# Kernel tuning notes

Measured on AMD Instinct MI355X. Metric: run time of the kernel, lower is better.

## Reference

```python
import jax, jax.numpy as jnp
import numpy as np

N_NODES = 100000
N_EDGES = 600000
IN_SIZE = 128
OUT_SIZE = 128
N_GRAPHS = 100
BN_EPS = 1e-5


def setup_inputs() -> dict:
    key = jax.random.key(0)
    ks = jax.random.split(key, 8)
    h = jax.random.normal(ks[0], (N_NODES, IN_SIZE), dtype=jnp.float32)
    norm = jax.random.uniform(ks[1], (N_NODES, 1), dtype=jnp.float32)
    src = jax.random.randint(ks[2], (N_EDGES,), 0, N_NODES, dtype=jnp.int32)
    dst = jax.random.randint(ks[3], (N_EDGES,), 0, N_NODES, dtype=jnp.int32)
    graph_ids = jnp.sort(jax.random.randint(ks[4], (N_NODES,), 0, N_GRAPHS, dtype=jnp.int32))
    # Linear + BatchNorm params
    W = jax.random.normal(ks[5], (IN_SIZE, OUT_SIZE), dtype=jnp.float32) / np.sqrt(IN_SIZE)
    b = jnp.zeros((OUT_SIZE,), dtype=jnp.float32)
    gamma = jnp.ones((OUT_SIZE,), dtype=jnp.float32)
    beta = jnp.zeros((OUT_SIZE,), dtype=jnp.float32)
    return {"h": h, "norm": norm, "W": W, "b": b, "gamma": gamma, "beta": beta,
            "src": src, "dst": dst, "graph_ids": graph_ids}


def reference(h, norm, W, b, gamma, beta, src, dst, graph_ids):
    # pre-normalize, scatter-sum over edges (copy_src + sum), post-normalize
    x = h * norm                                            # [N, in]
    agg = jax.ops.segment_sum(x[src], dst, num_segments=N_NODES)  # SpMM
    x = agg * norm
    # linear + relu
    x = jax.nn.relu(jnp.dot(x, W) + b)                      # [N, out]
    # BatchNorm1d (training-mode: batch mean, biased variance)
    mean = jnp.mean(x, axis=0)
    var = jnp.mean(jnp.square(x - mean), axis=0)
    x = (x - mean) * jax.lax.rsqrt(var + BN_EPS) * gamma + beta
    # sum_nodes pooling per graph
    phis = jax.ops.segment_sum(x, graph_ids, num_segments=N_GRAPHS)  # [G, out]
    return (x, phis)
```

## Files before the change

kernel.cpp:

```cpp
#include <hip/hip_runtime.h>
#include <hip/hip_bf16.h>

#define N_NODES 100000
#define N_PAD 100096
#define N_EDGES 600000
#define CH 128
#define N_GRAPHS 100
#define BN_EPS 1e-5f
#define NBUCKET 64
#define CAP 32
#define OVFCAP 8192
#define FILL_BLOCKS 586
#define PRESCALE_BLOCKS 6250

typedef __bf16 bf16x8 __attribute__((ext_vector_type(8)));
typedef float f32x4 __attribute__((ext_vector_type(4)));

__device__ __forceinline__ ushort f2bf(float f) {
    union { float f; unsigned u; } x; x.f = f;
    unsigned u = x.u;
    unsigned r = (u + 0x7fffu + ((u >> 16) & 1u)) >> 16;
    return (ushort)r;
}
__device__ __forceinline__ float bflo(unsigned p) { return __builtin_bit_cast(float, p << 16); }
__device__ __forceinline__ float bfhi(unsigned p) { return __builtin_bit_cast(float, p & 0xffff0000u); }

__global__ __launch_bounds__(256) void k_front(const int* __restrict__ src,
        const int* __restrict__ dst, const float* __restrict__ h,
        const float* __restrict__ norm, const float* __restrict__ W,
        int* __restrict__ cnt, int* __restrict__ ovfcur, int* __restrict__ ovf,
        int* __restrict__ esrc, ushort* __restrict__ xh, ushort* __restrict__ Wt) {
    unsigned bid = blockIdx.x;
    if (bid < FILL_BLOCKS) {
        int e0 = (bid * 256 + threadIdx.x) * 4;
        if (e0 < N_EDGES) {
            int4 d = *(const int4*)(dst + e0);
            int4 s = *(const int4*)(src + e0);
            int s0 = atomicAdd(&cnt[d.x], 1);
            int s1 = atomicAdd(&cnt[d.y], 1);
            int s2 = atomicAdd(&cnt[d.z], 1);
            int s3 = atomicAdd(&cnt[d.w], 1);
            if (s0 < CAP) esrc[d.x * CAP + s0] = s.x;
            else { int p = atomicAdd(ovfcur, 1); if (p < OVFCAP) { ovf[2*p] = d.x; ovf[2*p+1] = s.x; } }
            if (s1 < CAP) esrc[d.y * CAP + s1] = s.y;
            else { int p = atomicAdd(ovfcur, 1); if (p < OVFCAP) { ovf[2*p] = d.y; ovf[2*p+1] = s.y; } }
            if (s2 < CAP) esrc[d.z * CAP + s2] = s.z;
            else { int p = atomicAdd(ovfcur, 1); if (p < OVFCAP) { ovf[2*p] = d.z; ovf[2*p+1] = s.z; } }
            if (s3 < CAP) esrc[d.w * CAP + s3] = s.w;
            else { int p = atomicAdd(ovfcur, 1); if (p < OVFCAP) { ovf[2*p] = d.w; ovf[2*p+1] = s.w; } }
        }
    } else if (bid < FILL_BLOCKS + PRESCALE_BLOCKS) {
        int t = (bid - FILL_BLOCKS) * 256 + threadIdx.x;
        int n = t >> 4, c = (t & 15) << 3;
        float nm = norm[n];
        float4 a = *(const float4*)(h + (size_t)n * CH + c);
        float4 d = *(const float4*)(h + (size_t)n * CH + c + 4);
        uint4 o;
        o.x = (unsigned)f2bf(a.x * nm) | ((unsigned)f2bf(a.y * nm) << 16);
        o.y = (unsigned)f2bf(a.z * nm) | ((unsigned)f2bf(a.w * nm) << 16);
        o.z = (unsigned)f2bf(d.x * nm) | ((unsigned)f2bf(d.y * nm) << 16);
        o.w = (unsigned)f2bf(d.z * nm) | ((unsigned)f2bf(d.w * nm) << 16);
        *(uint4*)(xh + (size_t)n * CH + c) = o;
    } else {
        int t = (bid - FILL_BLOCKS - PRESCALE_BLOCKS) * 256 + threadIdx.x;
        int k = t >> 7, o = t & 127;
        Wt[o * CH + k] = f2bf(W[t]);
    }
}

__global__ __launch_bounds__(256) void k_gather(const ushort* __restrict__ xh,
        const float* __restrict__ norm, const int* __restrict__ cnt,
        const int* __restrict__ esrc, const int* __restrict__ ovfcur,
        const int* __restrict__ ovf, ushort* __restrict__ x2) {
    int t = blockIdx.x * 256 + threadIdx.x;
    int n = t >> 4;
    int c = (t & 15) << 3;
    if (n >= N_PAD) return;
    int e = 0;
    float nn = 0.f;
    if (n < N_NODES) { e = min(cnt[n], CAP); nn = norm[n]; }
    int base = n * CAP;
    float a0=0.f,a1=0.f,a2=0.f,a3=0.f,a4=0.f,a5=0.f,a6=0.f,a7=0.f;
    int j = 0;
    for (; j + 4 <= e; j += 4) {
        int s0 = esrc[base + j], s1 = esrc[base + j + 1];
        int s2 = esrc[base + j + 2], s3 = esrc[base + j + 3];
        uint4 v0 = *(const uint4*)(xh + (size_t)s0 * CH + c);
        uint4 v1 = *(const uint4*)(xh + (size_t)s1 * CH + c);
        uint4 v2 = *(const uint4*)(xh + (size_t)s2 * CH + c);
        uint4 v3 = *(const uint4*)(xh + (size_t)s3 * CH + c);
        a0 += bflo(v0.x) + bflo(v1.x) + bflo(v2.x) + bflo(v3.x);
        a1 += bfhi(v0.x) + bfhi(v1.x) + bfhi(v2.x) + bfhi(v3.x);
        a2 += bflo(v0.y) + bflo(v1.y) + bflo(v2.y) + bflo(v3.y);
        a3 += bfhi(v0.y) + bfhi(v1.y) + bfhi(v2.y) + bfhi(v3.y);
        a4 += bflo(v0.z) + bflo(v1.z) + bflo(v2.z) + bflo(v3.z);
        a5 += bfhi(v0.z) + bfhi(v1.z) + bfhi(v2.z) + bfhi(v3.z);
        a6 += bflo(v0.w) + bflo(v1.w) + bflo(v2.w) + bflo(v3.w);
        a7 += bfhi(v0.w) + bfhi(v1.w) + bfhi(v2.w) + bfhi(v3.w);
    }
    for (; j < e; j++) {
        int s = esrc[base + j];
        uint4 v = *(const uint4*)(xh + (size_t)s * CH + c);
        a0 += bflo(v.x); a1 += bfhi(v.x);
        a2 += bflo(v.y); a3 += bfhi(v.y);
        a4 += bflo(v.z); a5 += bfhi(v.z);
        a6 += bflo(v.w); a7 += bfhi(v.w);
    }
    if (n < N_NODES) {
        int no = *ovfcur;
        if (no > 0) {
            no = min(no, OVFCAP);
            for (int i = 0; i < no; i++) {
                if (ovf[2*i] == n) {
                    int s = ovf[2*i+1];
                    uint4 v = *(const uint4*)(xh + (size_t)s * CH + c);
                    a0 += bflo(v.x); a1 += bfhi(v.x);
                    a2 += bflo(v.y); a3 += bfhi(v.y);
                    a4 += bflo(v.z); a5 += bfhi(v.z);
                    a6 += bflo(v.w); a7 += bfhi(v.w);
                }
            }
        }
    }
    uint4 o;
    o.x = (unsigned)f2bf(a0 * nn) | ((unsigned)f2bf(a1 * nn) << 16);
    o.y = (unsigned)f2bf(a2 * nn) | ((unsigned)f2bf(a3 * nn) << 16);
    o.z = (unsigned)f2bf(a4 * nn) | ((unsigned)f2bf(a5 * nn) << 16);
    o.w = (unsigned)f2bf(a6 * nn) | ((unsigned)f2bf(a7 * nn) << 16);
    *(uint4*)(x2 + (size_t)n * CH + c) = o;
}

__global__ __launch_bounds__(256) void k_gemm(const ushort* __restrict__ x2,
        const ushort* __restrict__ Wt, const float* __restrict__ bias,
        ushort* __restrict__ y16, float* __restrict__ psum, float* __restrict__ psq) {
    __shared__ ushort ys[128 * CH];

    int tid = threadIdx.x;
    int w = tid >> 6, L = tid & 63;
    int c15 = L & 15, quad = L >> 4;
    size_t nb = (size_t)blockIdx.x * 128 + w * 32;

    const bf16x8* A0 = (const bf16x8*)(x2 + (nb + c15) * CH);
    const bf16x8* A1 = (const bf16x8*)(x2 + (nb + 16 + c15) * CH);

    f32x4 acc0[8] = {}, acc1[8] = {};
    #pragma unroll
    for (int kt = 0; kt < 4; kt++) {
        bf16x8 a0 = A0[kt * 4 + quad];
        bf16x8 a1 = A1[kt * 4 + quad];
        #pragma unroll
        for (int ot = 0; ot < 8; ot++) {
            bf16x8 b = *(const bf16x8*)(Wt + (size_t)(ot * 16 + c15) * CH + kt * 32 + quad * 8);
            acc0[ot] = __builtin_amdgcn_mfma_f32_16x16x32_bf16(a0, b, acc0[ot], 0, 0, 0);
            acc1[ot] = __builtin_amdgcn_mfma_f32_16x16x32_bf16(a1, b, acc1[ot], 0, 0, 0);
        }
    }

    float sA[8], qA[8];
    #pragma unroll
    for (int ot = 0; ot < 8; ot++) {
        int col = ot * 16 + c15;
        float bv = bias[col];
        float s_ = 0.f, q_ = 0.f;
        #pragma unroll
        for (int r = 0; r < 4; r++) {
            size_t n = nb + quad * 4 + r;
            float v = fmaxf(acc0[ot][r] + bv, 0.f);
            ys[(w * 32 + quad * 4 + r) * CH + col] = f2bf(v);
            if (n < N_NODES) { s_ += v; q_ += v * v; }
            size_t n2 = n + 16;
            float v2 = fmaxf(acc1[ot][r] + bv, 0.f);
            ys[(w * 32 + 16 + quad * 4 + r) * CH + col] = f2bf(v2);
            if (n2 < N_NODES) { s_ += v2; q_ += v2 * v2; }
        }
        sA[ot] = s_; qA[ot] = q_;
    }
    __syncthreads();

    {
        const uint4* ysv = (const uint4*)ys;
        uint4* out = (uint4*)(y16 + (size_t)blockIdx.x * 128 * CH);
        #pragma unroll
        for (int i = 0; i < 8; i++) out[tid + i * 256] = ysv[tid + i * 256];
    }
    __syncthreads();

    float* red = (float*)ys;
    #pragma unroll
    for (int ot = 0; ot < 8; ot++) {
        red[ot * 256 + tid] = sA[ot];
        red[2048 + ot * 256 + tid] = qA[ot];
    }
    __syncthreads();

    if (tid < 128) {
        int ot = tid >> 4, cc = tid & 15;
        int col = ot * 16 + cc;
        float S = 0.f, Q = 0.f;
        #pragma unroll
        for (int g = 0; g < 16; g++) {
            int sl = (g >> 2) * 64 + (g & 3) * 16 + cc;
            S += red[ot * 256 + sl];
            Q += red[2048 + ot * 256 + sl];
        }
        int bucket = blockIdx.x & (NBUCKET - 1);
        atomicAdd(&psum[bucket * CH + col], S);
        atomicAdd(&psq[bucket * CH + col], Q);
    }
}

__global__ void k_finalize(const float* __restrict__ psum, const float* __restrict__ psq,
        const float* __restrict__ gamma, const float* __restrict__ beta,
        float* __restrict__ scale, float* __restrict__ shift, float* __restrict__ phis) {
    int t = threadIdx.x;
    float S = 0.f, Q = 0.f;
    for (int g = 0; g < NBUCKET; g++) { S += psum[g * CH + t]; Q += psq[g * CH + t]; }
    const float invN = 1.f / (float)N_NODES;
    float mean = S * invN;
    float var  = Q * invN - mean * mean;
    float sc   = gamma[t] * rsqrtf(var + BN_EPS);
    scale[t] = sc;
    shift[t] = beta[t] - mean * sc;
    for (int i = t; i < N_GRAPHS * CH; i += 128) phis[i] = 0.f;
}

__global__ __launch_bounds__(256) void k_bnpool(const ushort* __restrict__ y16,
        const int* __restrict__ gids, const float* __restrict__ scale,
        const float* __restrict__ shift, float* __restrict__ xout,
        float* __restrict__ phis) {
    __shared__ float smP[16][CH];

    int tid = threadIdx.x;
    int cg = tid & 15, rl = tid >> 4;
    int c = cg * 8;
    int r0 = blockIdx.x * 256;
    int rbase = r0 + rl * 16;

    float4 sc0 = *(const float4*)(scale + c), sc1 = *(const float4*)(scale + c + 4);
    float4 sh0 = *(const float4*)(shift + c), sh1 = *(const float4*)(shift + c + 4);

    bool fast = (r0 + 255 < N_NODES) && (gids[r0] == gids[r0 + 255]);

    if (fast) {
        float4 p0 = make_float4(0.f,0.f,0.f,0.f), p1 = make_float4(0.f,0.f,0.f,0.f);
        for (int j = 0; j < 16; j++) {
            int r = rbase + j;
            uint4 v = *(const uint4*)(y16 + (size_t)r * CH + c);
            float4 f0, f1;
            f0.x = fmaf(bflo(v.x), sc0.x, sh0.x); f0.y = fmaf(bfhi(v.x), sc0.y, sh0.y);
            f0.z = fmaf(bflo(v.y), sc0.z, sh0.z); f0.w = fmaf(bfhi(v.y), sc0.w, sh0.w);
            f1.x = fmaf(bflo(v.z), sc1.x, sh1.x); f1.y = fmaf(bfhi(v.z), sc1.y, sh1.y);
            f1.z = fmaf(bflo(v.w), sc1.z, sh1.z); f1.w = fmaf(bfhi(v.w), sc1.w, sh1.w);
            *(float4*)(xout + (size_t)r * CH + c) = f0;
            *(float4*)(xout + (size_t)r * CH + c + 4) = f1;
            p0.x += f0.x; p0.y += f0.y; p0.z += f0.z; p0.w += f0.w;
            p1.x += f1.x; p1.y += f1.y; p1.z += f1.z; p1.w += f1.w;
        }
        *(float4*)&smP[rl][c] = p0;
        *(float4*)&smP[rl][c + 4] = p1;
        __syncthreads();
        if (tid < 128) {
            int g = gids[r0];
            float S = 0.f;
            #pragma unroll
            for (int k = 0; k < 16; k++) S += smP[k][tid];
            atomicAdd(&phis[(size_t)g * CH + tid], S);
        }
    } else {
        float p[8] = {};
        int gprev = -1;
        for (int j = 0; j < 16; j++) {
            int r = rbase + j;
            if (r >= N_NODES) break;
            int g = gids[r];
            if (g != gprev) {
                if (gprev >= 0) {
                    #pragma unroll
                    for (int k = 0; k < 8; k++) {
                        atomicAdd(&phis[(size_t)gprev * CH + c + k], p[k]);
                        p[k] = 0.f;
                    }
                }
                gprev = g;
            }
            uint4 v = *(const uint4*)(y16 + (size_t)r * CH + c);
            float f[8];
            f[0] = fmaf(bflo(v.x), sc0.x, sh0.x); f[1] = fmaf(bfhi(v.x), sc0.y, sh0.y);
            f[2] = fmaf(bflo(v.y), sc0.z, sh0.z); f[3] = fmaf(bfhi(v.y), sc0.w, sh0.w);
            f[4] = fmaf(bflo(v.z), sc1.x, sh1.x); f[5] = fmaf(bfhi(v.z), sc1.y, sh1.y);
            f[6] = fmaf(bflo(v.w), sc1.z, sh1.z); f[7] = fmaf(bfhi(v.w), sc1.w, sh1.w);
            *(float4*)(xout + (size_t)r * CH + c) = make_float4(f[0], f[1], f[2], f[3]);
            *(float4*)(xout + (size_t)r * CH + c + 4) = make_float4(f[4], f[5], f[6], f[7]);
            #pragma unroll
            for (int k = 0; k < 8; k++) p[k] += f[k];
        }
        if (gprev >= 0) {
            #pragma unroll
            for (int k = 0; k < 8; k++)
                atomicAdd(&phis[(size_t)gprev * CH + c + k], p[k]);
        }
    }
}

extern "C" void kernel_launch(void* const* d_in, const int* in_sizes, int n_in,
                              void* d_out, int out_size, void* d_ws, size_t ws_size,
                              hipStream_t stream)
{
    const float* h     = (const float*)d_in[0];
    const float* norm  = (const float*)d_in[1];
    const float* W     = (const float*)d_in[2];
    const float* b     = (const float*)d_in[3];
    const float* gamma = (const float*)d_in[4];
    const float* beta  = (const float*)d_in[5];
    const int*   src   = (const int*)d_in[6];
    const int*   dst   = (const int*)d_in[7];
    const int*   gids  = (const int*)d_in[8];

    float* x_out = (float*)d_out;
    float* phis  = x_out + (size_t)N_NODES * CH;

    ushort* xh   = (ushort*)d_ws;
    ushort* x2   = xh + (size_t)N_NODES * CH;
    ushort* y16  = x2 + (size_t)N_PAD * CH;
    ushort* Wt   = y16 + (size_t)N_PAD * CH;
    int*   cnt     = (int*)(Wt + CH * CH);
    float* psum    = (float*)(cnt + N_NODES);
    float* psq     = psum + NBUCKET * CH;
    int*   ovfcur  = (int*)(psq + NBUCKET * CH);
    int*   esrc    = ovfcur + 4;
    int*   ovf     = esrc + (size_t)N_NODES * CAP;
    float* scale   = (float*)(ovf + 2 * OVFCAP);
    float* shift   = scale + CH;

    hipMemsetAsync(cnt, 0, (size_t)(N_NODES + 2 * NBUCKET * CH + 4) * sizeof(int), stream);

    k_front<<<FILL_BLOCKS + PRESCALE_BLOCKS + 64, 256, 0, stream>>>(
        src, dst, h, norm, W, cnt, ovfcur, ovf, esrc, xh, Wt);
    k_gather<<<N_PAD / 16, 256, 0, stream>>>(xh, norm, cnt, esrc, ovfcur, ovf, x2);
    k_gemm<<<N_PAD / 128, 256, 0, stream>>>(x2, Wt, b, y16, psum, psq);
    k_finalize<<<1, 128, 0, stream>>>(psum, psq, gamma, beta, scale, shift, phis);
    k_bnpool<<<(N_NODES + 255) / 256, 256, 0, stream>>>(y16, gids, scale, shift, x_out, phis);
}
```

Before: 229.2 us.

## Apply linear layer before aggregation and fuse gather with bias, ReLU and BN stats

```diff
diff --git a/kernel.cpp b/kernel.cpp
--- a/kernel.cpp
+++ b/kernel.cpp
@@ -8,10 +8,13 @@
 #define N_GRAPHS 100
 #define BN_EPS 1e-5f
 #define NBUCKET 64
-#define CAP 32
+#define CAP 16
 #define OVFCAP 8192
 #define FILL_BLOCKS 586
-#define PRESCALE_BLOCKS 6250
+#define GEMM_BLOCKS 782
+#define GATHER_BLOCKS 1024
+#define ZERO_INTS (N_NODES + 2 * NBUCKET * CH + 4)
+#define ZERO_BLOCKS 455
 
 typedef __bf16 bf16x8 __attribute__((ext_vector_type(8)));
 typedef float f32x4 __attribute__((ext_vector_type(4)));
@@ -25,14 +28,47 @@
 __device__ __forceinline__ float bflo(unsigned p) { return __builtin_bit_cast(float, p << 16); }
 __device__ __forceinline__ float bfhi(unsigned p) { return __builtin_bit_cast(float, p & 0xffff0000u); }
 
+__global__ __launch_bounds__(256) void k_prep(const float* __restrict__ W,
+        int* __restrict__ zbase, ushort* __restrict__ Wt) {
+    unsigned bid = blockIdx.x;
+    if (bid < ZERO_BLOCKS) {
+        int i = bid * 256 + threadIdx.x;
+        if (i < ZERO_INTS) zbase[i] = 0;
+    } else {
+        int t = (bid - ZERO_BLOCKS) * 256 + threadIdx.x;
+        int k = t >> 7, o = t & 127;
+        Wt[o * CH + k] = f2bf(W[t]);
+    }
+}
+
+__device__ __forceinline__ bf16x8 mk_a(const float* __restrict__ hrow, int k,
+                                       float nm, bool valid) {
+    union { bf16x8 v; ushort u[8]; } r;
+    if (valid) {
+        float4 p = *(const float4*)(hrow + k);
+        float4 q = *(const float4*)(hrow + k + 4);
+        r.u[0] = f2bf(p.x * nm); r.u[1] = f2bf(p.y * nm);
+        r.u[2] = f2bf(p.z * nm); r.u[3] = f2bf(p.w * nm);
+        r.u[4] = f2bf(q.x * nm); r.u[5] = f2bf(q.y * nm);
+        r.u[6] = f2bf(q.z * nm); r.u[7] = f2bf(q.w * nm);
+    } else {
+        #pragma unroll
+        for (int i = 0; i < 8; i++) r.u[i] = 0;
+    }
+    return r.v;
+}
+
 __global__ __launch_bounds__(256) void k_front(const int* __restrict__ src,
         const int* __restrict__ dst, const float* __restrict__ h,
-        const float* __restrict__ norm, const float* __restrict__ W,
+        const float* __restrict__ norm, const ushort* __restrict__ Wt,
         int* __restrict__ cnt, int* __restrict__ ovfcur, int* __restrict__ ovf,
-        int* __restrict__ esrc, ushort* __restrict__ xh, ushort* __restrict__ Wt) {
+        int* __restrict__ esrc, ushort* __restrict__ z16) {
+    __shared__ ushort ys[128 * CH];
     unsigned bid = blockIdx.x;
+    int tid = threadIdx.x;
+
     if (bid < FILL_BLOCKS) {
-        int e0 = (bid * 256 + threadIdx.x) * 4;
+        int e0 = (bid * 256 + tid) * 4;
         if (e0 < N_EDGES) {
             int4 d = *(const int4*)(dst + e0);
             int4 s = *(const int4*)(src + e0);
@@ -49,71 +85,100 @@
             if (s3 < CAP) esrc[d.w * CAP + s3] = s.w;
             else { int p = atomicAdd(ovfcur, 1); if (p < OVFCAP) { ovf[2*p] = d.w; ovf[2*p+1] = s.w; } }
         }
-    } else if (bid < FILL_BLOCKS + PRESCALE_BLOCKS) {
-        int t = (bid - FILL_BLOCKS) * 256 + threadIdx.x;
-        int n = t >> 4, c = (t & 15) << 3;
-        float nm = norm[n];
-        float4 a = *(const float4*)(h + (size_t)n * CH + c);
-        float4 d = *(const float4*)(h + (size_t)n * CH + c + 4);
-        uint4 o;
-        o.x = (unsigned)f2bf(a.x * nm) | ((unsigned)f2bf(a.y * nm) << 16);
-        o.y = (unsigned)f2bf(a.z * nm) | ((unsigned)f2bf(a.w * nm) << 16);
-        o.z = (unsigned)f2bf(d.x * nm) | ((unsigned)f2bf(d.y * nm) << 16);
-        o.w = (unsigned)f2bf(d.z * nm) | ((unsigned)f2bf(d.w * nm) << 16);
-        *(uint4*)(xh + (size_t)n * CH + c) = o;
-    } else {
-        int t = (bid - FILL_BLOCKS - PRESCALE_BLOCKS) * 256 + threadIdx.x;
-        int k = t >> 7, o = t & 127;
-        Wt[o * CH + k] = f2bf(W[t]);
-    }
-}
-
-__global__ __launch_bounds__(256) void k_gather(const ushort* __restrict__ xh,
+        return;
+    }
+
+    int gb = bid - FILL_BLOCKS;
+    int w = tid >> 6, L = tid & 63;
+    int c15 = L & 15, quad = L >> 4;
+    int nb = gb * 128 + w * 32;
+    int r0 = nb + c15, r1 = nb + 16 + c15;
+    bool v0r = r0 < N_NODES, v1r = r1 < N_NODES;
+    float nm0 = v0r ? norm[r0] : 0.f;
+    float nm1 = v1r ? norm[r1] : 0.f;
+    const float* h0 = h + (size_t)r0 * CH;
+    const float* h1 = h + (size_t)r1 * CH;
+
+    f32x4 acc0[8] = {}, acc1[8] = {};
+    #pragma unroll
+    for (int kt = 0; kt < 4; kt++) {
+        int k = kt * 32 + quad * 8;
+        bf16x8 a0 = mk_a(h0, k, nm0, v0r);
+        bf16x8 a1 = mk_a(h1, k, nm1, v1r);
+        #pragma unroll
+        for (int ot = 0; ot < 8; ot++) {
+            bf16x8 b = *(const bf16x8*)(Wt + (size_t)(ot * 16 + c15) * CH + k);
+            acc0[ot] = __builtin_amdgcn_mfma_f32_16x16x32_bf16(a0, b, acc0[ot], 0, 0, 0);
+            acc1[ot] = __builtin_amdgcn_mfma_f32_16x16x32_bf16(a1, b, acc1[ot], 0, 0, 0);
+        }
+    }
+
+    #pragma unroll
+    for (int ot = 0; ot < 8; ot++) {
+        int col = ot * 16 + c15;
+        #pragma unroll
+        for (int r = 0; r < 4; r++) {
+            ys[(w * 32 + quad * 4 + r) * CH + col] = f2bf(acc0[ot][r]);
+            ys[(w * 32 + 16 + quad * 4 + r) * CH + col] = f2bf(acc1[ot][r]);
+        }
+    }
+    __syncthreads();
+    {
+        const uint4* ysv = (const uint4*)ys;
+        uint4* out = (uint4*)(z16 + (size_t)gb * 128 * CH);
+        #pragma unroll
+        for (int i = 0; i < 8; i++) out[tid + i * 256] = ysv[tid + i * 256];
+    }
+}
+
+__global__ __launch_bounds__(256) void k_gather(const ushort* __restrict__ z16,
         const float* __restrict__ norm, const int* __restrict__ cnt,
         const int* __restrict__ esrc, const int* __restrict__ ovfcur,
-        const int* __restrict__ ovf, ushort* __restrict__ x2) {
-    int t = blockIdx.x * 256 + threadIdx.x;
-    int n = t >> 4;
-    int c = (t & 15) << 3;
-    if (n >= N_PAD) return;
-    int e = 0;
-    float nn = 0.f;
-    if (n < N_NODES) { e = min(cnt[n], CAP); nn = norm[n]; }
-    int base = n * CAP;
-    float a0=0.f,a1=0.f,a2=0.f,a3=0.f,a4=0.f,a5=0.f,a6=0.f,a7=0.f;
-    int j = 0;
-    for (; j + 4 <= e; j += 4) {
-        int s0 = esrc[base + j], s1 = esrc[base + j + 1];
-        int s2 = esrc[base + j + 2], s3 = esrc[base + j + 3];
-        uint4 v0 = *(const uint4*)(xh + (size_t)s0 * CH + c);
-        uint4 v1 = *(const uint4*)(xh + (size_t)s1 * CH + c);
-        uint4 v2 = *(const uint4*)(xh + (size_t)s2 * CH + c);
-        uint4 v3 = *(const uint4*)(xh + (size_t)s3 * CH + c);
-        a0 += bflo(v0.x) + bflo(v1.x) + bflo(v2.x) + bflo(v3.x);
-        a1 += bfhi(v0.x) + bfhi(v1.x) + bfhi(v2.x) + bfhi(v3.x);
-        a2 += bflo(v0.y) + bflo(v1.y) + bflo(v2.y) + bflo(v3.y);
-        a3 += bfhi(v0.y) + bfhi(v1.y) + bfhi(v2.y) + bfhi(v3.y);
-        a4 += bflo(v0.z) + bflo(v1.z) + bflo(v2.z) + bflo(v3.z);
-        a5 += bfhi(v0.z) + bfhi(v1.z) + bfhi(v2.z) + bfhi(v3.z);
-        a6 += bflo(v0.w) + bflo(v1.w) + bflo(v2.w) + bflo(v3.w);
-        a7 += bfhi(v0.w) + bfhi(v1.w) + bfhi(v2.w) + bfhi(v3.w);
-    }
-    for (; j < e; j++) {
-        int s = esrc[base + j];
-        uint4 v = *(const uint4*)(xh + (size_t)s * CH + c);
-        a0 += bflo(v.x); a1 += bfhi(v.x);
-        a2 += bflo(v.y); a3 += bfhi(v.y);
-        a4 += bflo(v.z); a5 += bfhi(v.z);
-        a6 += bflo(v.w); a7 += bfhi(v.w);
-    }
-    if (n < N_NODES) {
-        int no = *ovfcur;
+        const int* __restrict__ ovf, const float* __restrict__ bias,
+        ushort* __restrict__ y16, float* __restrict__ psum, float* __restrict__ psq) {
+    __shared__ float sred[2][16][CH];
+
+    int tid = threadIdx.x;
+    int cg = tid & 15, rl = tid >> 4;
+    int c = cg * 8;
+    float4 b0 = *(const float4*)(bias + c), b1 = *(const float4*)(bias + c + 4);
+    float s8[8] = {}, q8[8] = {};
+    int no = min(*ovfcur, OVFCAP);
+
+    for (int n = blockIdx.x * 16 + rl; n < N_NODES; n += GATHER_BLOCKS * 16) {
+        int e = min(cnt[n], CAP);
+        float nn = norm[n];
+        int base = n * CAP;
+        float a0=0.f,a1=0.f,a2=0.f,a3=0.f,a4=0.f,a5=0.f,a6=0.f,a7=0.f;
+        int j = 0;
+        for (; j + 4 <= e; j += 4) {
+            int4 s4 = *(const int4*)(esrc + base + j);
+            uint4 v0 = *(const uint4*)(z16 + (size_t)s4.x * CH + c);
+            uint4 v1 = *(const uint4*)(z16 + (size_t)s4.y * CH + c);
+            uint4 v2 = *(const uint4*)(z16 + (size_t)s4.z * CH + c);
+            uint4 v3 = *(const uint4*)(z16 + (size_t)s4.w * CH + c);
+            a0 += bflo(v0.x) + bflo(v1.x) + bflo(v2.x) + bflo(v3.x);
+            a1 += bfhi(v0.x) + bfhi(v1.x) + bfhi(v2.x) + bfhi(v3.x);
+            a2 += bflo(v0.y) + bflo(v1.y) + bflo(v2.y) + bflo(v3.y);
+            a3 += bfhi(v0.y) + bfhi(v1.y) + bfhi(v2.y) + bfhi(v3.y);
+            a4 += bflo(v0.z) + bflo(v1.z) + bflo(v2.z) + bflo(v3.z);
+            a5 += bfhi(v0.z) + bfhi(v1.z) + bfhi(v2.z) + bfhi(v3.z);
+            a6 += bflo(v0.w) + bflo(v1.w) + bflo(v2.w) + bflo(v3.w);
+            a7 += bfhi(v0.w) + bfhi(v1.w) + bfhi(v2.w) + bfhi(v3.w);
+        }
+        for (; j < e; j++) {
+            int s = esrc[base + j];
+            uint4 v = *(const uint4*)(z16 + (size_t)s * CH + c);
+            a0 += bflo(v.x); a1 += bfhi(v.x);
+            a2 += bflo(v.y); a3 += bfhi(v.y);
+            a4 += bflo(v.z); a5 += bfhi(v.z);
+            a6 += bflo(v.w); a7 += bfhi(v.w);
+        }
         if (no > 0) {
-            no = min(no, OVFCAP);
             for (int i = 0; i < no; i++) {
                 if (ovf[2*i] == n) {
                     int s = ovf[2*i+1];
-                    uint4 v = *(const uint4*)(xh + (size_t)s * CH + c);
+                    uint4 v = *(const uint4*)(z16 + (size_t)s * CH + c);
                     a0 += bflo(v.x); a1 += bfhi(v.x);
                     a2 += bflo(v.y); a3 += bfhi(v.y);
                     a4 += bflo(v.z); a5 += bfhi(v.z);
@@ -121,91 +186,37 @@
                 }
             }
         }
-    }
-    uint4 o;
-    o.x = (unsigned)f2bf(a0 * nn) | ((unsigned)f2bf(a1 * nn) << 16);
-    o.y = (unsigned)f2bf(a2 * nn) | ((unsigned)f2bf(a3 * nn) << 16);
-    o.z = (unsigned)f2bf(a4 * nn) | ((unsigned)f2bf(a5 * nn) << 16);
-    o.w = (unsigned)f2bf(a6 * nn) | ((unsigned)f2bf(a7 * nn) << 16);
-    *(uint4*)(x2 + (size_t)n * CH + c) = o;
-}
-
-__global__ __launch_bounds__(256) void k_gemm(const ushort* __restrict__ x2,
-        const ushort* __restrict__ Wt, const float* __restrict__ bias,
-        ushort* __restrict__ y16, float* __restrict__ psum, float* __restrict__ psq) {
-    __shared__ ushort ys[128 * CH];
-
-    int tid = threadIdx.x;
-    int w = tid >> 6, L = tid & 63;
-    int c15 = L & 15, quad = L >> 4;
-    size_t nb = (size_t)blockIdx.x * 128 + w * 32;
-
-    const bf16x8* A0 = (const bf16x8*)(x2 + (nb + c15) * CH);
-    const bf16x8* A1 = (const bf16x8*)(x2 + (nb + 16 + c15) * CH);
-
-    f32x4 acc0[8] = {}, acc1[8] = {};
-    #pragma unroll
-    for (int kt = 0; kt < 4; kt++) {
-        bf16x8 a0 = A0[kt * 4 + quad];
-        bf16x8 a1 = A1[kt * 4 + quad];
-        #pragma unroll
-        for (int ot = 0; ot < 8; ot++) {
-            bf16x8 b = *(const bf16x8*)(Wt + (size_t)(ot * 16 + c15) * CH + kt * 32 + quad * 8);
-            acc0[ot] = __builtin_amdgcn_mfma_f32_16x16x32_bf16(a0, b, acc0[ot], 0, 0, 0);
-            acc1[ot] = __builtin_amdgcn_mfma_f32_16x16x32_bf16(a1, b, acc1[ot], 0, 0, 0);
-        }
-    }
-
-    float sA[8], qA[8];
-    #pragma unroll
-    for (int ot = 0; ot < 8; ot++) {
-        int col = ot * 16 + c15;
-        float bv = bias[col];
-        float s_ = 0.f, q_ = 0.f;
-        #pragma unroll
-        for (int r = 0; r < 4; r++) {
-            size_t n = nb + quad * 4 + r;
-            float v = fmaxf(acc0[ot][r] + bv, 0.f);
-            ys[(w * 32 + quad * 4 + r) * CH + col] = f2bf(v);
-            if (n < N_NODES) { s_ += v; q_ += v * v; }
-            size_t n2 = n + 16;
-            float v2 = fmaxf(acc1[ot][r] + bv, 0.f);
-            ys[(w * 32 + 16 + quad * 4 + r) * CH + col] = f2bf(v2);
-            if (n2 < N_NODES) { s_ += v2; q_ += v2 * v2; }
-        }
-        sA[ot] = s_; qA[ot] = q_;
-    }
+        float f[8];
+        f[0] = fmaxf(fmaf(a0, nn, b0.x), 0.f);
+        f[1] = fmaxf(fmaf(a1, nn, b0.y), 0.f);
+        f[2] = fmaxf(fmaf(a2, nn, b0.z), 0.f);
+        f[3] = fmaxf(fmaf(a3, nn, b0.w), 0.f);
+        f[4] = fmaxf(fmaf(a4, nn, b1.x), 0.f);
+        f[5] = fmaxf(fmaf(a5, nn, b1.y), 0.f);
+        f[6] = fmaxf(fmaf(a6, nn, b1.z), 0.f);
+        f[7] = fmaxf(fmaf(a7, nn, b1.w), 0.f);
+        uint4 o;
+        o.x = (unsigned)f2bf(f[0]) | ((unsigned)f2bf(f[1]) << 16);
+        o.y = (unsigned)f2bf(f[2]) | ((unsigned)f2bf(f[3]) << 16);
+        o.z = (unsigned)f2bf(f[4]) | ((unsigned)f2bf(f[5]) << 16);
+        o.w = (unsigned)f2bf(f[6]) | ((unsigned)f2bf(f[7]) << 16);
+        *(uint4*)(y16 + (size_t)n * CH + c) = o;
+        #pragma unroll
+        for (int k = 0; k < 8; k++) { s8[k] += f[k]; q8[k] += f[k] * f[k]; }
+    }
+
+    *(float4*)&sred[0][rl][c]     = make_float4(s8[0], s8[1], s8[2], s8[3]);
+    *(float4*)&sred[0][rl][c + 4] = make_float4(s8[4], s8[5], s8[6], s8[7]);
+    *(float4*)&sred[1][rl][c]     = make_float4(q8[0], q8[1], q8[2], q8[3]);
+    *(float4*)&sred[1][rl][c + 4] = make_float4(q8[4], q8[5], q8[6], q8[7]);
     __syncthreads();
-
-    {
-        const uint4* ysv = (const uint4*)ys;
-        uint4* out = (uint4*)(y16 + (size_t)blockIdx.x * 128 * CH);
-        #pragma unroll
-        for (int i = 0; i < 8; i++) out[tid + i * 256] = ysv[tid + i * 256];
-    }
-    __syncthreads();
-
-    float* red = (float*)ys;
-    #pragma unroll
-    for (int ot = 0; ot < 8; ot++) {
-        red[ot * 256 + tid] = sA[ot];
-        red[2048 + ot * 256 + tid] = qA[ot];
-    }
-    __syncthreads();
-
     if (tid < 128) {
-        int ot = tid >> 4, cc = tid & 15;
-        int col = ot * 16 + cc;
         float S = 0.f, Q = 0.f;
         #pragma unroll
-        for (int g = 0; g < 16; g++) {
-            int sl = (g >> 2) * 64 + (g & 3) * 16 + cc;
-            S += red[ot * 256 + sl];
-            Q += red[2048 + ot * 256 + sl];
-        }
+        for (int k = 0; k < 16; k++) { S += sred[0][k][tid]; Q += sred[1][k][tid]; }
         int bucket = blockIdx.x & (NBUCKET - 1);
-        atomicAdd(&psum[bucket * CH + col], S);
-        atomicAdd(&psq[bucket * CH + col], Q);
+        atomicAdd(&psum[bucket * CH + tid], S);
+        atomicAdd(&psq[bucket * CH + tid], Q);
     }
 }
 
@@ -319,9 +330,8 @@
     float* x_out = (float*)d_out;
     float* phis  = x_out + (size_t)N_NODES * CH;
 
-    ushort* xh   = (ushort*)d_ws;
-    ushort* x2   = xh + (size_t)N_NODES * CH;
-    ushort* y16  = x2 + (size_t)N_PAD * CH;
+    ushort* z16  = (ushort*)d_ws;
+    ushort* y16  = z16 + (size_t)N_PAD * CH;
     ushort* Wt   = y16 + (size_t)N_PAD * CH;
     int*   cnt     = (int*)(Wt + CH * CH);
     float* psum    = (float*)(cnt + N_NODES);
@@ -332,12 +342,11 @@
     float* scale   = (float*)(ovf + 2 * OVFCAP);
     float* shift   = scale + CH;
 
-    hipMemsetAsync(cnt, 0, (size_t)(N_NODES + 2 * NBUCKET * CH + 4) * sizeof(int), stream);
-
-    k_front<<<FILL_BLOCKS + PRESCALE_BLOCKS + 64, 256, 0, stream>>>(
-        src, dst, h, norm, W, cnt, ovfcur, ovf, esrc, xh, Wt);
-    k_gather<<<N_PAD / 16, 256, 0, stream>>>(xh, norm, cnt, esrc, ovfcur, ovf, x2);
-    k_gemm<<<N_PAD / 128, 256, 0, stream>>>(x2, Wt, b, y16, psum, psq);
+    k_prep<<<ZERO_BLOCKS + 64, 256, 0, stream>>>(W, cnt, Wt);
+    k_front<<<FILL_BLOCKS + GEMM_BLOCKS, 256, 0, stream>>>(
+        src, dst, h, norm, Wt, cnt, ovfcur, ovf, esrc, z16);
+    k_gather<<<GATHER_BLOCKS, 256, 0, stream>>>(
+        z16, norm, cnt, esrc, ovfcur, ovf, b, y16, psum, psq);
     k_finalize<<<1, 128, 0, stream>>>(psum, psq, gamma, beta, scale, shift, phis);
     k_bnpool<<<(N_NODES + 255) / 256, 256, 0, stream>>>(y16, gids, scale, shift, x_out, phis);
 }
```

New measurement: 229.6 us. No clear change (+0.2%).
